# Kernel optimization log

Hardware: AMD Instinct MI355X
Metric: run time of the kernel (lower is better)

## Reference

```python
import jax, jax.numpy as jnp
import numpy as np

B, S, H, NH = 1, 4096, 1024, 16
HD = H // NH  # 64


def _rope_tables(seq_len, dim):
    inv_freq = 1.0 / (10000.0 ** (np.arange(0, dim, 2, dtype=np.float32) / dim))
    t = np.arange(seq_len, dtype=np.float32)
    freqs = np.outer(t, inv_freq)                 # [S, dim/2]
    emb = np.concatenate([freqs, freqs], axis=-1)  # [S, dim]
    return jnp.asarray(np.cos(emb)), jnp.asarray(np.sin(emb))


def setup_inputs() -> dict:
    key = jax.random.key(0)
    ks = jax.random.split(key, 5)
    hidden_states = jax.random.normal(ks[0], (B, S, H), dtype=jnp.float32)
    scale = 1.0 / np.sqrt(H)
    Wq = jax.random.normal(ks[1], (H, H), dtype=jnp.float32) * scale
    Wk = jax.random.normal(ks[2], (H, H), dtype=jnp.float32) * scale
    Wv = jax.random.normal(ks[3], (H, H), dtype=jnp.float32) * scale
    Wo = jax.random.normal(ks[4], (H, H), dtype=jnp.float32) * scale
    cos, sin = _rope_tables(S, HD)
    # additive causal mask [1,1,S,S]
    causal = jnp.where(
        jnp.tril(jnp.ones((S, S), dtype=bool)), 0.0, jnp.float32(-1e9)
    )[None, None]
    return {
        "hidden_states": hidden_states,
        "cos": cos,
        "sin": sin,
        "attention_mask": causal,
        "Wq": Wq,
        "Wk": Wk,
        "Wv": Wv,
        "Wo": Wo,
    }


def _rotate_half(x):
    x1, x2 = jnp.split(x, 2, axis=-1)
    return jnp.concatenate([-x2, x1], axis=-1)


def _apply_rope(q, k, cos, sin):
    # q,k: [B,NH,S,HD]; cos/sin: [S,HD] -> broadcast [1,1,S,HD]
    cos = cos[None, None]
    sin = sin[None, None]
    q = q * cos + _rotate_half(q) * sin
    k = k * cos + _rotate_half(k) * sin
    return q, k


def reference(hidden_states, cos, sin, attention_mask, Wq, Wk, Wv, Wo):
    bsz, q_len, _ = hidden_states.shape
    q = hidden_states @ Wq.T
    k = hidden_states @ Wk.T
    v = hidden_states @ Wv.T
    # [B,S,H] -> [B,NH,S,HD]
    def split_heads(x):
        return x.reshape(bsz, q_len, NH, HD).transpose(0, 2, 1, 3)
    q, k, v = split_heads(q), split_heads(k), split_heads(v)
    q, k = _apply_rope(q, k, cos, sin)
    scores = jnp.einsum("bhqd,bhkd->bhqk", q, k) / jnp.sqrt(jnp.float32(HD))
    scores = scores + attention_mask
    attn = jax.nn.softmax(scores, axis=-1)
    out = jnp.einsum("bhqk,bhkd->bhqd", attn, v)
    out = out.transpose(0, 2, 1, 3).reshape(bsz, q_len, H)
    return out @ Wo.T
```

## Files before the change

kernel.cpp:

```cpp
#include <hip/hip_runtime.h>

#define S_LEN 4096
#define NHEADS 16
#define HD 64
#define HDIM 1024

typedef __attribute__((ext_vector_type(8))) __bf16 bf16x8;
typedef __attribute__((ext_vector_type(4))) float f32x4;
typedef __attribute__((ext_vector_type(4))) int i32x4;
typedef unsigned short u16;

static __device__ __forceinline__ u16 f2bu(float f) {
    unsigned u = __builtin_bit_cast(unsigned, f);
    u += 0x7FFFu + ((u >> 16) & 1u);
    return (u16)(u >> 16);
}
static __device__ __forceinline__ int pack_bf16(float lo, float hi) {
    return (int)__builtin_amdgcn_perm(__builtin_bit_cast(unsigned, hi),
                                      __builtin_bit_cast(unsigned, lo), 0x07060302u);
}
static __device__ __forceinline__ float fexp2(float x) {
    return __builtin_amdgcn_exp2f(x);
}

static __device__ __forceinline__ bf16x8 read_frag(const u16* lds, int row, int kbyte) {
    int c = kbyte ^ ((row & 7) << 4);
    return *reinterpret_cast<const bf16x8*>(reinterpret_cast<const char*>(lds) + row * 128 + c);
}
static __device__ __forceinline__ bf16x8 read_off(const u16* lds, int byteoff) {
    return *reinterpret_cast<const bf16x8*>(reinterpret_cast<const char*>(lds) + byteoff);
}

static __device__ __forceinline__ void stage_gll(const u16* __restrict__ src, const u16* lds, unsigned ldsbyte) {
    __builtin_amdgcn_global_load_lds(
        (const __attribute__((address_space(1))) void*)src,
        (__attribute__((address_space(3))) void*)(reinterpret_cast<const char*>(lds) + ldsbyte),
        16, 0, 0);
}

static __device__ __forceinline__ void softmax_gather(
    const f32x4* sf, float& l_part, bf16x8* pf, int lj, int lc)
{
    int pk[4][2];
#pragma unroll
    for (int nf = 0; nf < 4; ++nf) {
        float p0 = fexp2(sf[nf][0]);
        float p1 = fexp2(sf[nf][1]);
        float p2 = fexp2(sf[nf][2]);
        float p3 = fexp2(sf[nf][3]);
        l_part += (p0 + p1) + (p2 + p3);
        pk[nf][0] = pack_bf16(p0, p1);
        pk[nf][1] = pack_bf16(p2, p3);
    }
#pragma unroll
    for (int kb = 0; kb < 2; ++kb) {
        i32x4 u;
#pragma unroll
        for (int s = 0; s < 4; ++s) {
            int srcl = lc + (((2 * lj + (s >> 1)) & 3) << 4);
            int v0 = __shfl(pk[2 * kb][s & 1], srcl);
            int v1 = __shfl(pk[2 * kb + 1][s & 1], srcl);
            u[s] = (lj & 2) ? v1 : v0;
        }
        pf[kb] = __builtin_bit_cast(bf16x8, u);
    }
}

__global__ __launch_bounds__(256) void cvt_all(
    const float* __restrict__ X, const float* __restrict__ Wq, const float* __restrict__ Wk,
    const float* __restrict__ Wv, const float* __restrict__ Wo,
    u16* __restrict__ Xb, u16* __restrict__ Wqb, u16* __restrict__ Wkb,
    u16* __restrict__ Wvb, u16* __restrict__ Wob)
{
    int i = blockIdx.x * 256 + threadIdx.x;
    const float* src; u16* dst; int off;
    if (i < (1 << 20)) { src = X; dst = Xb; off = i; }
    else {
        int j = i - (1 << 20);
        int w = j >> 18; off = j & 0x3FFFF;
        src = (w == 0) ? Wq : (w == 1) ? Wk : (w == 2) ? Wv : Wo;
        dst = (w == 0) ? Wqb : (w == 1) ? Wkb : (w == 2) ? Wvb : Wob;
    }
    float4 v = reinterpret_cast<const float4*>(src)[off];
    ushort4 o;
    o.x = f2bu(v.x); o.y = f2bu(v.y); o.z = f2bu(v.z); o.w = f2bu(v.w);
    reinterpret_cast<ushort4*>(dst)[off] = o;
}

__global__ __launch_bounds__(256) void qkv_gemm(
    const u16* __restrict__ A,
    const u16* __restrict__ Wq, const u16* __restrict__ Wk, const u16* __restrict__ Wv,
    u16* __restrict__ Qb, u16* __restrict__ Kb, u16* __restrict__ VTb,
    const float* __restrict__ cosT, const float* __restrict__ sinT)
{
    __shared__ u16 At[128 * 64];
    __shared__ u16 Bt[128 * 64];
    const int z = blockIdx.z;
    const u16* W = (z == 0) ? Wq : (z == 1) ? Wk : Wv;
    const int tid = threadIdx.x;
    const int wid = tid >> 6, lane = tid & 63;
    const int wm = wid >> 1, wn = wid & 1;
    const int lj = lane >> 4, lc = lane & 15;
    const int m0 = blockIdx.x * 128, n0 = blockIdx.y * 128;

    f32x4 acc[4][4];
#pragma unroll
    for (int i = 0; i < 4; ++i)
#pragma unroll
        for (int j = 0; j < 4; ++j) acc[i][j] = 0.0f;

    for (int k0 = 0; k0 < HDIM; k0 += 64) {
        __syncthreads();
#pragma unroll
        for (int r = 0; r < 4; ++r) {
            int idx = (r << 8) + tid;
            int row = idx >> 3;
            int c = (idx & 7) << 4;
            int csw = c ^ ((row & 7) << 4);
            unsigned lb = (unsigned)(idx & ~63) << 4;
            stage_gll(A + (size_t)(m0 + row) * HDIM + k0 + (csw >> 1), At, lb);
            stage_gll(W + (size_t)(n0 + row) * HDIM + k0 + (csw >> 1), Bt, lb);
        }
        __syncthreads();
#pragma unroll
        for (int kb = 0; kb < 2; ++kb) {
            int kbyte = (kb << 6) + (lj << 4);
            bf16x8 af[4], bfr[4];
#pragma unroll
            for (int mf = 0; mf < 4; ++mf) af[mf] = read_frag(At, (wm << 6) + (mf << 4) + lc, kbyte);
#pragma unroll
            for (int nf = 0; nf < 4; ++nf) bfr[nf] = read_frag(Bt, (wn << 6) + (nf << 4) + lc, kbyte);
#pragma unroll
            for (int mf = 0; mf < 4; ++mf)
#pragma unroll
                for (int nf = 0; nf < 4; ++nf)
                    acc[mf][nf] = __builtin_amdgcn_mfma_f32_16x16x32_bf16(af[mf], bfr[nf], acc[mf][nf], 0, 0, 0);
        }
    }

    const int mrow0 = m0 + (wm << 6);
    const int ncol0 = n0 + (wn << 6);
    if (z == 2) {
#pragma unroll
        for (int mf = 0; mf < 4; ++mf)
#pragma unroll
            for (int nf = 0; nf < 4; ++nf)
#pragma unroll
                for (int j = 0; j < 4; ++j) {
                    int s = mrow0 + (mf << 4) + (lj << 2) + j;
                    int o = ncol0 + (nf << 4) + lc;
                    VTb[((size_t)(o >> 6) * HD + (o & 63)) * S_LEN + s] = f2bu(acc[mf][nf][j]);
                }
    } else {
        u16* outB = (z == 0) ? Qb : Kb;
        const float sc = (z == 0) ? 0.18033688011112042f : 1.0f;
#pragma unroll
        for (int mf = 0; mf < 4; ++mf) {
            float nv[4][4];
#pragma unroll
            for (int nf = 0; nf < 4; ++nf)
#pragma unroll
                for (int j = 0; j < 4; ++j) {
                    int s = mrow0 + (mf << 4) + (lj << 2) + j;
                    int o = ncol0 + (nf << 4) + lc;
                    int d = o & 63;
                    float x  = acc[mf][nf][j];
                    float xp = acc[mf][nf ^ 2][j];
                    float cv = cosT[(size_t)s * HD + d];
                    float sv = sinT[(size_t)s * HD + d];
                    float rot = (d < 32) ? -xp : xp;
                    nv[nf][j] = (x * cv + rot * sv) * sc;
                }
#pragma unroll
            for (int nf = 0; nf < 4; ++nf)
#pragma unroll
                for (int j = 0; j < 4; ++j) {
                    int s = mrow0 + (mf << 4) + (lj << 2) + j;
                    int o = ncol0 + (nf << 4) + lc;
                    outB[((size_t)(o >> 6) * S_LEN + s) * HD + (o & 63)] = f2bu(nv[nf][j]);
                }
        }
    }
}

__global__ __launch_bounds__(256) void wo_gemm(
    const u16* __restrict__ A, const u16* __restrict__ W, float* __restrict__ outF)
{
    __shared__ u16 At[128 * 64];
    __shared__ u16 Bt[64 * 64];
    const int tid = threadIdx.x;
    const int wid = tid >> 6, lane = tid & 63;
    const int wm = wid >> 1, wn = wid & 1;
    const int lj = lane >> 4, lc = lane & 15;
    const int m0 = blockIdx.x * 128, n0 = blockIdx.y * 64;

    f32x4 acc[4][2];
#pragma unroll
    for (int i = 0; i < 4; ++i)
#pragma unroll
        for (int j = 0; j < 2; ++j) acc[i][j] = 0.0f;

    for (int k0 = 0; k0 < HDIM; k0 += 64) {
        __syncthreads();
#pragma unroll
        for (int r = 0; r < 4; ++r) {
            int idx = (r << 8) + tid;
            int row = idx >> 3;
            int c = (idx & 7) << 4;
            int csw = c ^ ((row & 7) << 4);
            unsigned lb = (unsigned)(idx & ~63) << 4;
            stage_gll(A + (size_t)(m0 + row) * HDIM + k0 + (csw >> 1), At, lb);
            if (r < 2)
                stage_gll(W + (size_t)(n0 + row) * HDIM + k0 + (csw >> 1), Bt, lb);
        }
        __syncthreads();
#pragma unroll
        for (int kb = 0; kb < 2; ++kb) {
            int kbyte = (kb << 6) + (lj << 4);
            bf16x8 af[4], bfr[2];
#pragma unroll
            for (int mf = 0; mf < 4; ++mf) af[mf] = read_frag(At, (wm << 6) + (mf << 4) + lc, kbyte);
#pragma unroll
            for (int nf = 0; nf < 2; ++nf) bfr[nf] = read_frag(Bt, (wn << 5) + (nf << 4) + lc, kbyte);
#pragma unroll
            for (int mf = 0; mf < 4; ++mf)
#pragma unroll
                for (int nf = 0; nf < 2; ++nf)
                    acc[mf][nf] = __builtin_amdgcn_mfma_f32_16x16x32_bf16(af[mf], bfr[nf], acc[mf][nf], 0, 0, 0);
        }
    }

    const int mrow0 = m0 + (wm << 6);
    const int ncol0 = n0 + (wn << 5);
#pragma unroll
    for (int mf = 0; mf < 4; ++mf)
#pragma unroll
        for (int nf = 0; nf < 2; ++nf)
#pragma unroll
            for (int j = 0; j < 4; ++j) {
                int s = mrow0 + (mf << 4) + (lj << 2) + j;
                int o = ncol0 + (nf << 4) + lc;
                outF[(size_t)s * HDIM + o] = acc[mf][nf][j];
            }
}

__global__ __launch_bounds__(256, 2) void attn_fwd(
    const u16* __restrict__ Q, const u16* __restrict__ K,
    const u16* __restrict__ VT, u16* __restrict__ AO)
{
    __shared__ u16 Kt[2][128 * 64];
    __shared__ u16 Vt[2][2][64 * 64];

    const int tid = threadIdx.x;
    const int wid = tid >> 6, lane = tid & 63;
    const int lj = lane >> 4, lc = lane & 15;

    const int lid = blockIdx.x;
    const int x = lid & 7, g = lid >> 3;
    const int h = (x << 1) | (g >> 5);
    const int j = g & 31;

    const u16* Qh = Q + (size_t)h * S_LEN * HD;

    const int srow = tid >> 3;
    const int csw  = ((tid & 7) << 4) ^ ((srow & 7) << 4);
    const u16* kbase = K  + (size_t)h * S_LEN * HD + (size_t)srow * HD + (csw >> 1);
    const u16* vbase = VT + (size_t)h * HD * S_LEN + (size_t)srow * S_LEN + (csw >> 1);
    const unsigned lb = (unsigned)(tid & ~63) << 4;

#define SK(buf, hf, t) do { \
        const u16* p_ = kbase + (size_t)(t) * 64 * HD; \
        stage_gll(p_,           (const u16*)Kt[buf] + (hf) * 4096, lb); \
        stage_gll(p_ + 32 * HD, (const u16*)Kt[buf] + (hf) * 4096, lb + 4096); \
    } while (0)
#define SV(buf, hf, t) do { \
        const u16* p_ = vbase + (t) * 64; \
        stage_gll(p_,              (const u16*)Vt[buf][hf], lb); \
        stage_gll(p_ + 32 * S_LEN, (const u16*)Vt[buf][hf], lb + 4096); \
    } while (0)

    int foff[2][4];
#pragma unroll
    for (int kb = 0; kb < 2; ++kb)
#pragma unroll
        for (int nf = 0; nf < 4; ++nf) {
            int row = (nf << 4) + lc;
            foff[kb][nf] = row * 128 + (((kb << 6) + (lj << 4)) ^ ((row & 7) << 4));
        }

#pragma unroll 1
    for (int phase = 0; phase < 2; ++phase) {
        const int qt = phase ? j : 63 - j;
        const int qbase = qt * 64 + wid * 16;
        const int nsteps = qt + 1;

        bf16x8 qB[2];
#pragma unroll
        for (int kb = 0; kb < 2; ++kb)
            qB[kb] = *reinterpret_cast<const bf16x8*>(
                Qh + (size_t)(qbase + lc) * HD + (kb << 5) + (lj << 3));

        f32x4 accO[4];
        float l0 = 0.0f;
#pragma unroll
        for (int df = 0; df < 4; ++df) accO[df] = 0.0f;

        bf16x8 pf[2], vf[2][4];

        auto compute = [&](int t, const u16* KtH, const u16* VtH) {
            bf16x8 kf[2][4];
#pragma unroll
            for (int kb = 0; kb < 2; ++kb)
#pragma unroll
                for (int nf = 0; nf < 4; ++nf)
                    kf[kb][nf] = read_off(KtH, foff[kb][nf]);

            f32x4 sf[4];
#pragma unroll
            for (int nf = 0; nf < 4; ++nf) sf[nf] = 0.0f;

            __builtin_amdgcn_s_setprio(1);
#pragma unroll
            for (int kb = 0; kb < 2; ++kb)
#pragma unroll
                for (int nf = 0; nf < 4; ++nf)
                    sf[nf] = __builtin_amdgcn_mfma_f32_16x16x32_bf16(kf[kb][nf], qB[kb], sf[nf], 0, 0, 0);
            if (t >= 1) {
#pragma unroll
                for (int kb = 0; kb < 2; ++kb)
#pragma unroll
                    for (int df = 0; df < 4; ++df)
                        accO[df] = __builtin_amdgcn_mfma_f32_16x16x32_bf16(pf[kb], vf[kb][df], accO[df], 0, 0, 0);
            }
            __builtin_amdgcn_s_setprio(0);

#pragma unroll
            for (int kb = 0; kb < 2; ++kb)
#pragma unroll
                for (int df = 0; df < 4; ++df)
                    vf[kb][df] = read_off(VtH, foff[kb][df]);

            if (t == qt) {
                int qg = qbase + lc;
                int kv0 = t << 6;
#pragma unroll
                for (int nf = 0; nf < 4; ++nf)
#pragma unroll
                    for (int jj = 0; jj < 4; ++jj) {
                        int kvg = kv0 + (nf << 4) + (lj << 2) + jj;
                        if (kvg > qg) sf[nf][jj] = -1e30f;
                    }
            }
            softmax_gather(sf, l0, pf, lj, lc);
        };

        SK(0, 0, 0); SV(0, 0, 0);
        if (nsteps > 1) { SK(0, 1, 1); SV(0, 1, 1); }
        __syncthreads();

        const int nmac = (nsteps + 1) >> 1;
        int cur = 0;
        for (int m = 0; m < nmac; ++m) {
            const int t2 = 2 * m + 2, t3 = 2 * m + 3;
            if (t2 < nsteps) { SK(cur ^ 1, 0, t2); SV(cur ^ 1, 0, t2); }
            if (t3 < nsteps) { SK(cur ^ 1, 1, t3); SV(cur ^ 1, 1, t3); }

            compute(2 * m, (const u16*)Kt[cur], (const u16*)Vt[cur][0]);
            if (2 * m + 1 < nsteps)
                compute(2 * m + 1, (const u16*)Kt[cur] + 4096, (const u16*)Vt[cur][1]);

            __syncthreads();
            cur ^= 1;
        }

#pragma unroll
        for (int kb = 0; kb < 2; ++kb)
#pragma unroll
            for (int df = 0; df < 4; ++df)
                accO[df] = __builtin_amdgcn_mfma_f32_16x16x32_bf16(pf[kb], vf[kb][df], accO[df], 0, 0, 0);

        l0 += __shfl_xor(l0, 16); l0 += __shfl_xor(l0, 32);
        float lr[4];
#pragma unroll
        for (int jj = 0; jj < 4; ++jj) lr[jj] = __shfl(l0, (lj << 2) + jj);
#pragma unroll
        for (int df = 0; df < 4; ++df)
#pragma unroll
            for (int jj = 0; jj < 4; ++jj) {
                int s = qbase + (lj << 2) + jj;
                int d = (df << 4) + lc;
                AO[(size_t)s * HDIM + h * HD + d] = f2bu(accO[df][jj] / lr[jj]);
            }
    }
#undef SK
#undef SV
}

extern "C" void kernel_launch(void* const* d_in, const int* in_sizes, int n_in,
                              void* d_out, int out_size, void* d_ws, size_t ws_size,
                              hipStream_t stream) {
    const float* hidden = (const float*)d_in[0];
    const float* cosT   = (const float*)d_in[1];
    const float* sinT   = (const float*)d_in[2];
    const float* Wq = (const float*)d_in[4];
    const float* Wk = (const float*)d_in[5];
    const float* Wv = (const float*)d_in[6];
    const float* Wo = (const float*)d_in[7];
    float* out = (float*)d_out;

    char* ws = (char*)d_ws;
    u16* Xb  = (u16*)(ws);
    u16* Wqb = (u16*)(ws + (size_t)( 8 << 20));
    u16* Wkb = (u16*)(ws + (size_t)(10 << 20));
    u16* Wvb = (u16*)(ws + (size_t)(12 << 20));
    u16* Wob = (u16*)(ws + (size_t)(14 << 20));
    u16* Qb  = (u16*)(ws + (size_t)(16 << 20));
    u16* Kb  = (u16*)(ws + (size_t)(24 << 20));
    u16* VTb = (u16*)(ws + (size_t)(32 << 20));
    u16* AOb = (u16*)(ws + (size_t)(40 << 20));

    cvt_all<<<8192, 256, 0, stream>>>(hidden, Wq, Wk, Wv, Wo, Xb, Wqb, Wkb, Wvb, Wob);

    qkv_gemm<<<dim3(S_LEN / 128, HDIM / 128, 3), 256, 0, stream>>>(
        Xb, Wqb, Wkb, Wvb, Qb, Kb, VTb, cosT, sinT);

    attn_fwd<<<dim3(512), 256, 0, stream>>>(Qb, Kb, VTb, AOb);

    wo_gemm<<<dim3(S_LEN / 128, HDIM / 64), 256, 0, stream>>>(AOb, Wob, out);
}
```

Measured before the change: 161.2 us.

## Interleave two KV tiles per macro-step in the causal attention inner loop

Replaces the per-tile compute lambda with a manually unrolled body that processes two KV tiles (A and B) together. It batches the K fragment loads and QK^T MFMAs for both tiles, then runs the deferred PV MFMAs for both previous tiles, loads V for both, and applies masks and softmax. The goal is more independent MFMA work between LDS reads and softmax, to hide latency and raise matrix-unit utilisation. The cost is roughly double the live fragment registers, which may lower occupancy or cause spills. An inactive B tile is handled with zeroed P fragments, so it still issues MFMAs on zeros.

```diff
diff --git a/kernel.cpp b/kernel.cpp
--- a/kernel.cpp
+++ b/kernel.cpp
@@ -305,54 +305,20 @@
 #pragma unroll
         for (int df = 0; df < 4; ++df) accO[df] = 0.0f;
 
-        bf16x8 pf[2], vf[2][4];
-
-        auto compute = [&](int t, const u16* KtH, const u16* VtH) {
-            bf16x8 kf[2][4];
-#pragma unroll
-            for (int kb = 0; kb < 2; ++kb)
-#pragma unroll
-                for (int nf = 0; nf < 4; ++nf)
-                    kf[kb][nf] = read_off(KtH, foff[kb][nf]);
-
-            f32x4 sf[4];
-#pragma unroll
-            for (int nf = 0; nf < 4; ++nf) sf[nf] = 0.0f;
-
-            __builtin_amdgcn_s_setprio(1);
-#pragma unroll
-            for (int kb = 0; kb < 2; ++kb)
-#pragma unroll
-                for (int nf = 0; nf < 4; ++nf)
-                    sf[nf] = __builtin_amdgcn_mfma_f32_16x16x32_bf16(kf[kb][nf], qB[kb], sf[nf], 0, 0, 0);
-            if (t >= 1) {
-#pragma unroll
-                for (int kb = 0; kb < 2; ++kb)
-#pragma unroll
-                    for (int df = 0; df < 4; ++df)
-                        accO[df] = __builtin_amdgcn_mfma_f32_16x16x32_bf16(pf[kb], vf[kb][df], accO[df], 0, 0, 0);
-            }
-            __builtin_amdgcn_s_setprio(0);
-
-#pragma unroll
-            for (int kb = 0; kb < 2; ++kb)
-#pragma unroll
-                for (int df = 0; df < 4; ++df)
-                    vf[kb][df] = read_off(VtH, foff[kb][df]);
-
-            if (t == qt) {
-                int qg = qbase + lc;
-                int kv0 = t << 6;
-#pragma unroll
-                for (int nf = 0; nf < 4; ++nf)
-#pragma unroll
-                    for (int jj = 0; jj < 4; ++jj) {
-                        int kvg = kv0 + (nf << 4) + (lj << 2) + jj;
-                        if (kvg > qg) sf[nf][jj] = -1e30f;
-                    }
-            }
-            softmax_gather(sf, l0, pf, lj, lc);
-        };
+        bf16x8 pfA[2], pfB[2], vfA[2][4], vfB[2][4];
+        {
+            i32x4 z = {0, 0, 0, 0};
+#pragma unroll
+            for (int kb = 0; kb < 2; ++kb) {
+                pfA[kb] = __builtin_bit_cast(bf16x8, z);
+                pfB[kb] = __builtin_bit_cast(bf16x8, z);
+#pragma unroll
+                for (int df = 0; df < 4; ++df) {
+                    vfA[kb][df] = __builtin_bit_cast(bf16x8, z);
+                    vfB[kb][df] = __builtin_bit_cast(bf16x8, z);
+                }
+            }
+        }
 
         SK(0, 0, 0); SV(0, 0, 0);
         if (nsteps > 1) { SK(0, 1, 1); SV(0, 1, 1); }
@@ -365,9 +331,100 @@
             if (t2 < nsteps) { SK(cur ^ 1, 0, t2); SV(cur ^ 1, 0, t2); }
             if (t3 < nsteps) { SK(cur ^ 1, 1, t3); SV(cur ^ 1, 1, t3); }
 
-            compute(2 * m, (const u16*)Kt[cur], (const u16*)Vt[cur][0]);
-            if (2 * m + 1 < nsteps)
-                compute(2 * m + 1, (const u16*)Kt[cur] + 4096, (const u16*)Vt[cur][1]);
+            const int tA = 2 * m, tB = 2 * m + 1;
+            const bool actB = (tB < nsteps);
+            const u16* KtA = (const u16*)Kt[cur];
+            const u16* KtB = (const u16*)Kt[cur] + 4096;
+            const u16* VtA = (const u16*)Vt[cur][0];
+            const u16* VtB = (const u16*)Vt[cur][1];
+
+            bf16x8 kfA[2][4], kfB[2][4];
+#pragma unroll
+            for (int kb = 0; kb < 2; ++kb)
+#pragma unroll
+                for (int nf = 0; nf < 4; ++nf)
+                    kfA[kb][nf] = read_off(KtA, foff[kb][nf]);
+            if (actB) {
+#pragma unroll
+                for (int kb = 0; kb < 2; ++kb)
+#pragma unroll
+                    for (int nf = 0; nf < 4; ++nf)
+                        kfB[kb][nf] = read_off(KtB, foff[kb][nf]);
+            }
+
+            f32x4 sfA[4], sfB[4];
+#pragma unroll
+            for (int nf = 0; nf < 4; ++nf) { sfA[nf] = 0.0f; sfB[nf] = 0.0f; }
+
+            __builtin_amdgcn_s_setprio(1);
+#pragma unroll
+            for (int kb = 0; kb < 2; ++kb)
+#pragma unroll
+                for (int nf = 0; nf < 4; ++nf)
+                    sfA[nf] = __builtin_amdgcn_mfma_f32_16x16x32_bf16(kfA[kb][nf], qB[kb], sfA[nf], 0, 0, 0);
+            if (actB) {
+#pragma unroll
+                for (int kb = 0; kb < 2; ++kb)
+#pragma unroll
+                    for (int nf = 0; nf < 4; ++nf)
+                        sfB[nf] = __builtin_amdgcn_mfma_f32_16x16x32_bf16(kfB[kb][nf], qB[kb], sfB[nf], 0, 0, 0);
+            }
+#pragma unroll
+            for (int kb = 0; kb < 2; ++kb)
+#pragma unroll
+                for (int df = 0; df < 4; ++df)
+                    accO[df] = __builtin_amdgcn_mfma_f32_16x16x32_bf16(pfA[kb], vfA[kb][df], accO[df], 0, 0, 0);
+#pragma unroll
+            for (int kb = 0; kb < 2; ++kb)
+#pragma unroll
+                for (int df = 0; df < 4; ++df)
+                    accO[df] = __builtin_amdgcn_mfma_f32_16x16x32_bf16(pfB[kb], vfB[kb][df], accO[df], 0, 0, 0);
+            __builtin_amdgcn_s_setprio(0);
+
+#pragma unroll
+            for (int kb = 0; kb < 2; ++kb)
+#pragma unroll
+                for (int df = 0; df < 4; ++df)
+                    vfA[kb][df] = read_off(VtA, foff[kb][df]);
+            if (actB) {
+#pragma unroll
+                for (int kb = 0; kb < 2; ++kb)
+#pragma unroll
+                    for (int df = 0; df < 4; ++df)
+                        vfB[kb][df] = read_off(VtB, foff[kb][df]);
+            }
+
+            if (tA == qt) {
+                int qg = qbase + lc;
+                int kv0 = tA << 6;
+#pragma unroll
+                for (int nf = 0; nf < 4; ++nf)
+#pragma unroll
+                    for (int jj = 0; jj < 4; ++jj) {
+                        int kvg = kv0 + (nf << 4) + (lj << 2) + jj;
+                        if (kvg > qg) sfA[nf][jj] = -1e30f;
+                    }
+            }
+            if (actB && tB == qt) {
+                int qg = qbase + lc;
+                int kv0 = tB << 6;
+#pragma unroll
+                for (int nf = 0; nf < 4; ++nf)
+#pragma unroll
+                    for (int jj = 0; jj < 4; ++jj) {
+                        int kvg = kv0 + (nf << 4) + (lj << 2) + jj;
+                        if (kvg > qg) sfB[nf][jj] = -1e30f;
+                    }
+            }
+
+            softmax_gather(sfA, l0, pfA, lj, lc);
+            if (actB) {
+                softmax_gather(sfB, l0, pfB, lj, lc);
+            } else {
+                i32x4 z = {0, 0, 0, 0};
+                pfB[0] = __builtin_bit_cast(bf16x8, z);
+                pfB[1] = __builtin_bit_cast(bf16x8, z);
+            }
 
             __syncthreads();
             cur ^= 1;
@@ -377,7 +434,12 @@
         for (int kb = 0; kb < 2; ++kb)
 #pragma unroll
             for (int df = 0; df < 4; ++df)
-                accO[df] = __builtin_amdgcn_mfma_f32_16x16x32_bf16(pf[kb], vf[kb][df], accO[df], 0, 0, 0);
+                accO[df] = __builtin_amdgcn_mfma_f32_16x16x32_bf16(pfA[kb], vfA[kb][df], accO[df], 0, 0, 0);
+#pragma unroll
+        for (int kb = 0; kb < 2; ++kb)
+#pragma unroll
+            for (int df = 0; df < 4; ++df)
+                accO[df] = __builtin_amdgcn_mfma_f32_16x16x32_bf16(pfB[kb], vfB[kb][df], accO[df], 0, 0, 0);
 
         l0 += __shfl_xor(l0, 16); l0 += __shfl_xor(l0, 32);
         float lr[4];
```

Measured after the change: 163.8 us. Within noise of the previous version (+1.6%).

## Process 128-row query tiles per block with two 16-row subtiles per wave

Applied to the files above, without the earlier changes.

Each block now handles one 128-row query tile (32 rows per wave, two MFMA subtiles) instead of two 64-row tiles processed in sequential phases. K/V fragments loaded from LDS are reused across both query subtiles, which halves LDS reads and staging traffic per unit of work. Load balance across blocks comes from mapping the tile index so that heads alternate between forward and reversed order, rather than pairing a short and a long tile inside one block. The change raises register pressure (doubled accumulators, scores and P fragments), which may spill at the existing launch bounds of 2 blocks per CU, and it leaves fewer blocks per head.

```diff
diff --git a/kernel.cpp b/kernel.cpp
--- a/kernel.cpp
+++ b/kernel.cpp
@@ -257,8 +257,11 @@
 
     const int lid = blockIdx.x;
     const int x = lid & 7, g = lid >> 3;
-    const int h = (x << 1) | (g >> 5);
-    const int j = g & 31;
+    const int a = g >> 5, c = g & 31;
+    const int qt = a ? (31 - c) : c;
+    const int h = (x << 1) | a;
+    const int qbase = qt * 128 + wid * 32;
+    const int nsteps = 2 * qt + 2;
 
     const u16* Qh = Q + (size_t)h * S_LEN * HD;
 
@@ -288,108 +291,121 @@
             foff[kb][nf] = row * 128 + (((kb << 6) + (lj << 4)) ^ ((row & 7) << 4));
         }
 
-#pragma unroll 1
-    for (int phase = 0; phase < 2; ++phase) {
-        const int qt = phase ? j : 63 - j;
-        const int qbase = qt * 64 + wid * 16;
-        const int nsteps = qt + 1;
-
-        bf16x8 qB[2];
+    bf16x8 qB[2][2];
+#pragma unroll
+    for (int s = 0; s < 2; ++s)
 #pragma unroll
         for (int kb = 0; kb < 2; ++kb)
-            qB[kb] = *reinterpret_cast<const bf16x8*>(
-                Qh + (size_t)(qbase + lc) * HD + (kb << 5) + (lj << 3));
-
-        f32x4 accO[4];
-        float l0 = 0.0f;
-#pragma unroll
-        for (int df = 0; df < 4; ++df) accO[df] = 0.0f;
-
-        bf16x8 pf[2], vf[2][4];
-
-        auto compute = [&](int t, const u16* KtH, const u16* VtH) {
-            bf16x8 kf[2][4];
+            qB[s][kb] = *reinterpret_cast<const bf16x8*>(
+                Qh + (size_t)(qbase + (s << 4) + lc) * HD + (kb << 5) + (lj << 3));
+
+    f32x4 accO[2][4];
+    float l0[2] = {0.0f, 0.0f};
+#pragma unroll
+    for (int s = 0; s < 2; ++s)
+#pragma unroll
+        for (int df = 0; df < 4; ++df) accO[s][df] = 0.0f;
+
+    bf16x8 pf[2][2], vf[2][4];
+
+    auto compute = [&](int t, const u16* KtH, const u16* VtH) {
+        bf16x8 kf[2][4];
+#pragma unroll
+        for (int kb = 0; kb < 2; ++kb)
+#pragma unroll
+            for (int nf = 0; nf < 4; ++nf)
+                kf[kb][nf] = read_off(KtH, foff[kb][nf]);
+
+        f32x4 sf[2][4];
+#pragma unroll
+        for (int s = 0; s < 2; ++s)
+#pragma unroll
+            for (int nf = 0; nf < 4; ++nf) sf[s][nf] = 0.0f;
+
+        __builtin_amdgcn_s_setprio(1);
+#pragma unroll
+        for (int kb = 0; kb < 2; ++kb)
+#pragma unroll
+            for (int nf = 0; nf < 4; ++nf) {
+                sf[0][nf] = __builtin_amdgcn_mfma_f32_16x16x32_bf16(kf[kb][nf], qB[0][kb], sf[0][nf], 0, 0, 0);
+                sf[1][nf] = __builtin_amdgcn_mfma_f32_16x16x32_bf16(kf[kb][nf], qB[1][kb], sf[1][nf], 0, 0, 0);
+            }
+        if (t >= 1) {
 #pragma unroll
             for (int kb = 0; kb < 2; ++kb)
 #pragma unroll
-                for (int nf = 0; nf < 4; ++nf)
-                    kf[kb][nf] = read_off(KtH, foff[kb][nf]);
-
-            f32x4 sf[4];
-#pragma unroll
-            for (int nf = 0; nf < 4; ++nf) sf[nf] = 0.0f;
-
-            __builtin_amdgcn_s_setprio(1);
-#pragma unroll
-            for (int kb = 0; kb < 2; ++kb)
-#pragma unroll
-                for (int nf = 0; nf < 4; ++nf)
-                    sf[nf] = __builtin_amdgcn_mfma_f32_16x16x32_bf16(kf[kb][nf], qB[kb], sf[nf], 0, 0, 0);
-            if (t >= 1) {
-#pragma unroll
-                for (int kb = 0; kb < 2; ++kb)
-#pragma unroll
-                    for (int df = 0; df < 4; ++df)
-                        accO[df] = __builtin_amdgcn_mfma_f32_16x16x32_bf16(pf[kb], vf[kb][df], accO[df], 0, 0, 0);
-            }
-            __builtin_amdgcn_s_setprio(0);
-
-#pragma unroll
-            for (int kb = 0; kb < 2; ++kb)
-#pragma unroll
-                for (int df = 0; df < 4; ++df)
-                    vf[kb][df] = read_off(VtH, foff[kb][df]);
-
-            if (t == qt) {
-                int qg = qbase + lc;
-                int kv0 = t << 6;
+                for (int df = 0; df < 4; ++df) {
+                    accO[0][df] = __builtin_amdgcn_mfma_f32_16x16x32_bf16(pf[0][kb], vf[kb][df], accO[0][df], 0, 0, 0);
+                    accO[1][df] = __builtin_amdgcn_mfma_f32_16x16x32_bf16(pf[1][kb], vf[kb][df], accO[1][df], 0, 0, 0);
+                }
+        }
+        __builtin_amdgcn_s_setprio(0);
+
+#pragma unroll
+        for (int kb = 0; kb < 2; ++kb)
+#pragma unroll
+            for (int df = 0; df < 4; ++df)
+                vf[kb][df] = read_off(VtH, foff[kb][df]);
+
+        if (t >= 2 * qt) {
+            int kv0 = t << 6;
+#pragma unroll
+            for (int s = 0; s < 2; ++s) {
+                int qg = qbase + (s << 4) + lc;
 #pragma unroll
                 for (int nf = 0; nf < 4; ++nf)
 #pragma unroll
                     for (int jj = 0; jj < 4; ++jj) {
                         int kvg = kv0 + (nf << 4) + (lj << 2) + jj;
-                        if (kvg > qg) sf[nf][jj] = -1e30f;
+                        if (kvg > qg) sf[s][nf][jj] = -1e30f;
                     }
             }
-            softmax_gather(sf, l0, pf, lj, lc);
-        };
-
-        SK(0, 0, 0); SV(0, 0, 0);
-        if (nsteps > 1) { SK(0, 1, 1); SV(0, 1, 1); }
+        }
+
+        softmax_gather(sf[0], l0[0], pf[0], lj, lc);
+        softmax_gather(sf[1], l0[1], pf[1], lj, lc);
+    };
+
+    SK(0, 0, 0); SV(0, 0, 0);
+    SK(0, 1, 1); SV(0, 1, 1);
+    __syncthreads();
+
+    const int nmac = nsteps >> 1;
+    int cur = 0;
+    for (int m = 0; m < nmac; ++m) {
+        const int t2 = 2 * m + 2, t3 = 2 * m + 3;
+        if (t2 < nsteps) { SK(cur ^ 1, 0, t2); SV(cur ^ 1, 0, t2); }
+        if (t3 < nsteps) { SK(cur ^ 1, 1, t3); SV(cur ^ 1, 1, t3); }
+
+        compute(2 * m, (const u16*)Kt[cur], (const u16*)Vt[cur][0]);
+        compute(2 * m + 1, (const u16*)Kt[cur] + 4096, (const u16*)Vt[cur][1]);
+
         __syncthreads();
-
-        const int nmac = (nsteps + 1) >> 1;
-        int cur = 0;
-        for (int m = 0; m < nmac; ++m) {
-            const int t2 = 2 * m + 2, t3 = 2 * m + 3;
-            if (t2 < nsteps) { SK(cur ^ 1, 0, t2); SV(cur ^ 1, 0, t2); }
-            if (t3 < nsteps) { SK(cur ^ 1, 1, t3); SV(cur ^ 1, 1, t3); }
-
-            compute(2 * m, (const u16*)Kt[cur], (const u16*)Vt[cur][0]);
-            if (2 * m + 1 < nsteps)
-                compute(2 * m + 1, (const u16*)Kt[cur] + 4096, (const u16*)Vt[cur][1]);
-
-            __syncthreads();
-            cur ^= 1;
-        }
-
-#pragma unroll
-        for (int kb = 0; kb < 2; ++kb)
-#pragma unroll
-            for (int df = 0; df < 4; ++df)
-                accO[df] = __builtin_amdgcn_mfma_f32_16x16x32_bf16(pf[kb], vf[kb][df], accO[df], 0, 0, 0);
-
-        l0 += __shfl_xor(l0, 16); l0 += __shfl_xor(l0, 32);
+        cur ^= 1;
+    }
+
+#pragma unroll
+    for (int kb = 0; kb < 2; ++kb)
+#pragma unroll
+        for (int df = 0; df < 4; ++df) {
+            accO[0][df] = __builtin_amdgcn_mfma_f32_16x16x32_bf16(pf[0][kb], vf[kb][df], accO[0][df], 0, 0, 0);
+            accO[1][df] = __builtin_amdgcn_mfma_f32_16x16x32_bf16(pf[1][kb], vf[kb][df], accO[1][df], 0, 0, 0);
+        }
+
+#pragma unroll
+    for (int s = 0; s < 2; ++s) {
+        float lp = l0[s];
+        lp += __shfl_xor(lp, 16); lp += __shfl_xor(lp, 32);
         float lr[4];
 #pragma unroll
-        for (int jj = 0; jj < 4; ++jj) lr[jj] = __shfl(l0, (lj << 2) + jj);
+        for (int jj = 0; jj < 4; ++jj) lr[jj] = __shfl(lp, (lj << 2) + jj);
 #pragma unroll
         for (int df = 0; df < 4; ++df)
 #pragma unroll
             for (int jj = 0; jj < 4; ++jj) {
-                int s = qbase + (lj << 2) + jj;
+                int sq = qbase + (s << 4) + (lj << 2) + jj;
                 int d = (df << 4) + lc;
-                AO[(size_t)s * HDIM + h * HD + d] = f2bu(accO[df][jj] / lr[jj]);
+                AO[(size_t)sq * HDIM + h * HD + d] = f2bu(accO[s][df][jj] / lr[jj]);
             }
     }
 #undef SK
```

Result: slower. 165.0 us (+2.3%).

## Drop V LDS staging, use 16x16x16 MFMA for PV, one q-tile per block

Applied to the files above, without the earlier changes.

The PV product switches to the 16x16x16 bf16 MFMA so the softmax probabilities can be used in their native accumulator layout, which removes the cross-lane shuffle gather. V fragments are now loaded directly from global memory into registers instead of being staged through LDS, which frees shared memory. The two-phase balanced loop is split into separate blocks (1024 blocks, launch bounds raised to 4) to increase occupancy. The cost is uncoalesced 8-byte global V loads with no LDS reuse, plus a loss of per-block load balancing, since each block now handles a single causal tile whose work varies.

```diff
diff --git a/kernel.cpp b/kernel.cpp
--- a/kernel.cpp
+++ b/kernel.cpp
@@ -8,6 +8,8 @@
 typedef __attribute__((ext_vector_type(8))) __bf16 bf16x8;
 typedef __attribute__((ext_vector_type(4))) float f32x4;
 typedef __attribute__((ext_vector_type(4))) int i32x4;
+typedef __attribute__((ext_vector_type(2))) int i32x2;
+typedef __attribute__((ext_vector_type(4))) short s16x4;
 typedef unsigned short u16;
 
 static __device__ __forceinline__ u16 f2bu(float f) {
@@ -21,6 +23,15 @@
 }
 static __device__ __forceinline__ float fexp2(float x) {
     return __builtin_amdgcn_exp2f(x);
+}
+
+static __device__ __forceinline__ f32x4 mfma16(s16x4 a, s16x4 b, f32x4 c) {
+#if __has_builtin(__builtin_amdgcn_mfma_f32_16x16x16bf16_1k)
+    return __builtin_amdgcn_mfma_f32_16x16x16bf16_1k(a, b, c, 0, 0, 0);
+#else
+    asm("v_mfma_f32_16x16x16_bf16 %0, %1, %2, %0" : "+v"(c) : "v"(a), "v"(b));
+    return c;
+#endif
 }
 
 static __device__ __forceinline__ bf16x8 read_frag(const u16* lds, int row, int kbyte) {
@@ -38,10 +49,9 @@
         16, 0, 0);
 }
 
-static __device__ __forceinline__ void softmax_gather(
-    const f32x4* sf, float& l_part, bf16x8* pf, int lj, int lc)
+static __device__ __forceinline__ void softmax_pack(
+    const f32x4* sf, float& l_part, s16x4* pk)
 {
-    int pk[4][2];
 #pragma unroll
     for (int nf = 0; nf < 4; ++nf) {
         float p0 = fexp2(sf[nf][0]);
@@ -49,20 +59,10 @@
         float p2 = fexp2(sf[nf][2]);
         float p3 = fexp2(sf[nf][3]);
         l_part += (p0 + p1) + (p2 + p3);
-        pk[nf][0] = pack_bf16(p0, p1);
-        pk[nf][1] = pack_bf16(p2, p3);
-    }
-#pragma unroll
-    for (int kb = 0; kb < 2; ++kb) {
-        i32x4 u;
-#pragma unroll
-        for (int s = 0; s < 4; ++s) {
-            int srcl = lc + (((2 * lj + (s >> 1)) & 3) << 4);
-            int v0 = __shfl(pk[2 * kb][s & 1], srcl);
-            int v1 = __shfl(pk[2 * kb + 1][s & 1], srcl);
-            u[s] = (lj & 2) ? v1 : v0;
-        }
-        pf[kb] = __builtin_bit_cast(bf16x8, u);
+        i32x2 w;
+        w[0] = pack_bf16(p0, p1);
+        w[1] = pack_bf16(p2, p3);
+        pk[nf] = __builtin_bit_cast(s16x4, w);
     }
 }
 
@@ -244,12 +244,11 @@
             }
 }
 
-__global__ __launch_bounds__(256, 2) void attn_fwd(
+__global__ __launch_bounds__(256, 4) void attn_fwd(
     const u16* __restrict__ Q, const u16* __restrict__ K,
     const u16* __restrict__ VT, u16* __restrict__ AO)
 {
     __shared__ u16 Kt[2][128 * 64];
-    __shared__ u16 Vt[2][2][64 * 64];
 
     const int tid = threadIdx.x;
     const int wid = tid >> 6, lane = tid & 63;
@@ -257,15 +256,17 @@
 
     const int lid = blockIdx.x;
     const int x = lid & 7, g = lid >> 3;
-    const int h = (x << 1) | (g >> 5);
-    const int j = g & 31;
+    const int a = g >> 6, c = g & 63;
+    const int qt = a ? (63 - c) : c;
+    const int h = (x << 1) | a;
+    const int qbase = qt * 64 + wid * 16;
+    const int nsteps = qt + 1;
 
     const u16* Qh = Q + (size_t)h * S_LEN * HD;
 
     const int srow = tid >> 3;
     const int csw  = ((tid & 7) << 4) ^ ((srow & 7) << 4);
-    const u16* kbase = K  + (size_t)h * S_LEN * HD + (size_t)srow * HD + (csw >> 1);
-    const u16* vbase = VT + (size_t)h * HD * S_LEN + (size_t)srow * S_LEN + (csw >> 1);
+    const u16* kbase = K + (size_t)h * S_LEN * HD + (size_t)srow * HD + (csw >> 1);
     const unsigned lb = (unsigned)(tid & ~63) << 4;
 
 #define SK(buf, hf, t) do { \
@@ -273,11 +274,6 @@
         stage_gll(p_,           (const u16*)Kt[buf] + (hf) * 4096, lb); \
         stage_gll(p_ + 32 * HD, (const u16*)Kt[buf] + (hf) * 4096, lb + 4096); \
     } while (0)
-#define SV(buf, hf, t) do { \
-        const u16* p_ = vbase + (t) * 64; \
-        stage_gll(p_,              (const u16*)Vt[buf][hf], lb); \
-        stage_gll(p_ + 32 * S_LEN, (const u16*)Vt[buf][hf], lb + 4096); \
-    } while (0)
 
     int foff[2][4];
 #pragma unroll
@@ -287,113 +283,109 @@
             int row = (nf << 4) + lc;
             foff[kb][nf] = row * 128 + (((kb << 6) + (lj << 4)) ^ ((row & 7) << 4));
         }
-
-#pragma unroll 1
-    for (int phase = 0; phase < 2; ++phase) {
-        const int qt = phase ? j : 63 - j;
-        const int qbase = qt * 64 + wid * 16;
-        const int nsteps = qt + 1;
-
-        bf16x8 qB[2];
+    const u16* vb[4];
+#pragma unroll
+    for (int df = 0; df < 4; ++df)
+        vb[df] = VT + (size_t)h * HD * S_LEN + (size_t)((df << 4) + lc) * S_LEN + (lj << 2);
+
+    bf16x8 qB[2];
+#pragma unroll
+    for (int kb = 0; kb < 2; ++kb)
+        qB[kb] = *reinterpret_cast<const bf16x8*>(
+            Qh + (size_t)(qbase + lc) * HD + (kb << 5) + (lj << 3));
+
+    f32x4 accO[4];
+    float l0 = 0.0f;
+#pragma unroll
+    for (int df = 0; df < 4; ++df) accO[df] = 0.0f;
+
+    s16x4 pk[4], vf64[4][4];
+
+    auto compute = [&](int t, const u16* KtH) {
+        bf16x8 kf[2][4];
 #pragma unroll
         for (int kb = 0; kb < 2; ++kb)
-            qB[kb] = *reinterpret_cast<const bf16x8*>(
-                Qh + (size_t)(qbase + lc) * HD + (kb << 5) + (lj << 3));
-
-        f32x4 accO[4];
-        float l0 = 0.0f;
-#pragma unroll
-        for (int df = 0; df < 4; ++df) accO[df] = 0.0f;
-
-        bf16x8 pf[2], vf[2][4];
-
-        auto compute = [&](int t, const u16* KtH, const u16* VtH) {
-            bf16x8 kf[2][4];
-#pragma unroll
-            for (int kb = 0; kb < 2; ++kb)
-#pragma unroll
-                for (int nf = 0; nf < 4; ++nf)
-                    kf[kb][nf] = read_off(KtH, foff[kb][nf]);
-
-            f32x4 sf[4];
-#pragma unroll
-            for (int nf = 0; nf < 4; ++nf) sf[nf] = 0.0f;
-
-            __builtin_amdgcn_s_setprio(1);
-#pragma unroll
-            for (int kb = 0; kb < 2; ++kb)
-#pragma unroll
-                for (int nf = 0; nf < 4; ++nf)
-                    sf[nf] = __builtin_amdgcn_mfma_f32_16x16x32_bf16(kf[kb][nf], qB[kb], sf[nf], 0, 0, 0);
-            if (t >= 1) {
-#pragma unroll
-                for (int kb = 0; kb < 2; ++kb)
-#pragma unroll
-                    for (int df = 0; df < 4; ++df)
-                        accO[df] = __builtin_amdgcn_mfma_f32_16x16x32_bf16(pf[kb], vf[kb][df], accO[df], 0, 0, 0);
-            }
-            __builtin_amdgcn_s_setprio(0);
-
-#pragma unroll
-            for (int kb = 0; kb < 2; ++kb)
+#pragma unroll
+            for (int nf = 0; nf < 4; ++nf)
+                kf[kb][nf] = read_off(KtH, foff[kb][nf]);
+
+        f32x4 sf[4];
+#pragma unroll
+        for (int nf = 0; nf < 4; ++nf) sf[nf] = 0.0f;
+
+        __builtin_amdgcn_s_setprio(1);
+#pragma unroll
+        for (int kb = 0; kb < 2; ++kb)
+#pragma unroll
+            for (int nf = 0; nf < 4; ++nf)
+                sf[nf] = __builtin_amdgcn_mfma_f32_16x16x32_bf16(kf[kb][nf], qB[kb], sf[nf], 0, 0, 0);
+        if (t >= 1) {
+#pragma unroll
+            for (int nf = 0; nf < 4; ++nf)
 #pragma unroll
                 for (int df = 0; df < 4; ++df)
-                    vf[kb][df] = read_off(VtH, foff[kb][df]);
-
-            if (t == qt) {
-                int qg = qbase + lc;
-                int kv0 = t << 6;
-#pragma unroll
-                for (int nf = 0; nf < 4; ++nf)
-#pragma unroll
-                    for (int jj = 0; jj < 4; ++jj) {
-                        int kvg = kv0 + (nf << 4) + (lj << 2) + jj;
-                        if (kvg > qg) sf[nf][jj] = -1e30f;
-                    }
-            }
-            softmax_gather(sf, l0, pf, lj, lc);
-        };
-
-        SK(0, 0, 0); SV(0, 0, 0);
-        if (nsteps > 1) { SK(0, 1, 1); SV(0, 1, 1); }
+                    accO[df] = mfma16(pk[nf], vf64[nf][df], accO[df]);
+        }
+        __builtin_amdgcn_s_setprio(0);
+
+        const int kv0 = t << 6;
+#pragma unroll
+        for (int nf = 0; nf < 4; ++nf)
+#pragma unroll
+            for (int df = 0; df < 4; ++df)
+                vf64[nf][df] = *reinterpret_cast<const s16x4*>(vb[df] + kv0 + (nf << 4));
+
+        if (t == qt) {
+            int qg = qbase + lc;
+#pragma unroll
+            for (int nf = 0; nf < 4; ++nf)
+#pragma unroll
+                for (int jj = 0; jj < 4; ++jj) {
+                    int kvg = kv0 + (nf << 4) + (lj << 2) + jj;
+                    if (kvg > qg) sf[nf][jj] = -1e30f;
+                }
+        }
+        softmax_pack(sf, l0, pk);
+    };
+
+    SK(0, 0, 0);
+    if (nsteps > 1) SK(0, 1, 1);
+    __syncthreads();
+
+    const int nmac = (nsteps + 1) >> 1;
+    int cur = 0;
+    for (int m = 0; m < nmac; ++m) {
+        const int t2 = 2 * m + 2, t3 = 2 * m + 3;
+        if (t2 < nsteps) SK(cur ^ 1, 0, t2);
+        if (t3 < nsteps) SK(cur ^ 1, 1, t3);
+
+        compute(2 * m, (const u16*)Kt[cur]);
+        if (2 * m + 1 < nsteps)
+            compute(2 * m + 1, (const u16*)Kt[cur] + 4096);
+
         __syncthreads();
-
-        const int nmac = (nsteps + 1) >> 1;
-        int cur = 0;
-        for (int m = 0; m < nmac; ++m) {
-            const int t2 = 2 * m + 2, t3 = 2 * m + 3;
-            if (t2 < nsteps) { SK(cur ^ 1, 0, t2); SV(cur ^ 1, 0, t2); }
-            if (t3 < nsteps) { SK(cur ^ 1, 1, t3); SV(cur ^ 1, 1, t3); }
-
-            compute(2 * m, (const u16*)Kt[cur], (const u16*)Vt[cur][0]);
-            if (2 * m + 1 < nsteps)
-                compute(2 * m + 1, (const u16*)Kt[cur] + 4096, (const u16*)Vt[cur][1]);
-
-            __syncthreads();
-            cur ^= 1;
-        }
-
-#pragma unroll
-        for (int kb = 0; kb < 2; ++kb)
-#pragma unroll
-            for (int df = 0; df < 4; ++df)
-                accO[df] = __builtin_amdgcn_mfma_f32_16x16x32_bf16(pf[kb], vf[kb][df], accO[df], 0, 0, 0);
-
-        l0 += __shfl_xor(l0, 16); l0 += __shfl_xor(l0, 32);
-        float lr[4];
-#pragma unroll
-        for (int jj = 0; jj < 4; ++jj) lr[jj] = __shfl(l0, (lj << 2) + jj);
+        cur ^= 1;
+    }
+
+#pragma unroll
+    for (int nf = 0; nf < 4; ++nf)
 #pragma unroll
         for (int df = 0; df < 4; ++df)
-#pragma unroll
-            for (int jj = 0; jj < 4; ++jj) {
-                int s = qbase + (lj << 2) + jj;
-                int d = (df << 4) + lc;
-                AO[(size_t)s * HDIM + h * HD + d] = f2bu(accO[df][jj] / lr[jj]);
-            }
-    }
+            accO[df] = mfma16(pk[nf], vf64[nf][df], accO[df]);
+
+    l0 += __shfl_xor(l0, 16); l0 += __shfl_xor(l0, 32);
+    float lr[4];
+#pragma unroll
+    for (int jj = 0; jj < 4; ++jj) lr[jj] = __shfl(l0, (lj << 2) + jj);
+#pragma unroll
+    for (int df = 0; df < 4; ++df)
+#pragma unroll
+        for (int jj = 0; jj < 4; ++jj) {
+            int s = qbase + (lj << 2) + jj;
+            int d = (df << 4) + lc;
+            AO[(size_t)s * HDIM + h * HD + d] = f2bu(accO[df][jj] / lr[jj]);
+        }
 #undef SK
-#undef SV
 }
 
 extern "C" void kernel_launch(void* const* d_in, const int* in_sizes, int n_in,
@@ -424,7 +416,7 @@
     qkv_gemm<<<dim3(S_LEN / 128, HDIM / 128, 3), 256, 0, stream>>>(
         Xb, Wqb, Wkb, Wvb, Qb, Kb, VTb, cosT, sinT);
 
-    attn_fwd<<<dim3(512), 256, 0, stream>>>(Qb, Kb, VTb, AOb);
+    attn_fwd<<<dim3(1024), 256, 0, stream>>>(Qb, Kb, VTb, AOb);
 
     wo_gemm<<<dim3(S_LEN / 128, HDIM / 64), 256, 0, stream>>>(AOb, Wob, out);
 }
```

Result: slower. 328.9 us (+104.0%).
